# Optimization experiments

Measured on AMD Instinct MI355X. Metric: run time of the kernel, lower is better.

The kernel has to match this reference:

```python
import jax, jax.numpy as jnp
import numpy as np

NUM_NETWORKS = 1024
IN_FEATURES = 32
OUT_FEATURES = 32
POINTS_PER_NET = 128
TOTAL_POINTS = NUM_NETWORKS * POINTS_PER_NET  # 131072


def setup_inputs() -> dict:
    key = jax.random.key(0)
    k1, k2, k3 = jax.random.split(key, 3)
    x = jax.random.normal(k1, (TOTAL_POINTS, IN_FEATURES), dtype=jnp.float32)
    # per-network weight matrices [N, in, out] and biases [N, out]
    weights = jax.random.normal(k2, (NUM_NETWORKS, IN_FEATURES, OUT_FEATURES), dtype=jnp.float32) * 0.1
    biases = jax.random.normal(k3, (NUM_NETWORKS, OUT_FEATURES), dtype=jnp.float32) * 0.1
    # contiguous point counts per network (static/uniform here, matching sum == TOTAL_POINTS)
    batch_size_per_network = jnp.full((NUM_NETWORKS,), POINTS_PER_NET, dtype=jnp.int32)
    return {"x": x, "weights": weights, "biases": biases,
            "batch_size_per_network": batch_size_per_network}


def reference(x, weights, biases, batch_size_per_network):
    # Grouped batched matmul: points are laid out contiguously per network.
    # seg[t] = network id owning point t.
    n = weights.shape[0]
    total = x.shape[0]
    seg = jnp.repeat(jnp.arange(n, dtype=jnp.int32), batch_size_per_network,
                     total_repeat_length=total)  # [total]
    # y_t = x_t @ W[seg_t] + b[seg_t]
    w_t = weights[seg]                     # [total, in, out] (gathered per point)
    y = jnp.einsum('ti,tio->to', x, w_t) + biases[seg]
    return y
```

## Files before the change

### kernel.cpp

```cpp
#include <hip/hip_runtime.h>


#define NT 64

__global__ __launch_bounds__(NT) void mnl_kernel(
    const float* __restrict__ x,
    const float* __restrict__ w,
    const float* __restrict__ bias,
    const int* __restrict__ cnt,
    float* __restrict__ y)
{
    __shared__ float xT[32][NT];
    __shared__ float Wl[32][32];

    const int b = blockIdx.x;
    const int n = b >> 1;
    const int h = b & 1;
    const int t = threadIdx.x;

    const float4* __restrict__ wg = reinterpret_cast<const float4*>(w + (size_t)n * 1024);
    const float4 wr0 = wg[t];
    const float4 wr1 = wg[t + 64];
    const float4 wr2 = wg[t + 128];
    const float4 wr3 = wg[t + 192];

    const int o0 = (t & 7) * 4;
    const int p0 = (t >> 3) * 8;

    const float4 b4 = *reinterpret_cast<const float4*>(bias + (size_t)n * 32 + o0);

    int s = 0;
    for (int j = t; j < n; j += NT) s += cnt[j];
    #pragma unroll
    for (int off = 32; off > 0; off >>= 1) s += __shfl_xor(s, off, 64);
    const int base  = s;
    const int count = cnt[n];

    {
        float4* wl4 = reinterpret_cast<float4*>(&Wl[0][0]);
        wl4[t]       = wr0;
        wl4[t + 64]  = wr1;
        wl4[t + 128] = wr2;
        wl4[t + 192] = wr3;
    }

    for (int pc = h * NT; pc < count; pc += 2 * NT) {
        const int p = pc + t;
        float4 rr[8];
        if (p < count) {
            const float4* __restrict__ xg =
                reinterpret_cast<const float4*>(x + (size_t)(base + p) * 32);
            #pragma unroll
            for (int k = 0; k < 8; ++k) rr[k] = xg[k];
        } else {
            #pragma unroll
            for (int k = 0; k < 8; ++k) rr[k] = make_float4(0.f, 0.f, 0.f, 0.f);
        }

        __syncthreads();

        #pragma unroll
        for (int k = 0; k < 8; ++k) {
            xT[4 * k + 0][t] = rr[k].x;
            xT[4 * k + 1][t] = rr[k].y;
            xT[4 * k + 2][t] = rr[k].z;
            xT[4 * k + 3][t] = rr[k].w;
        }

        __syncthreads();

        float acc[8][4] = {};
        #pragma unroll
        for (int i = 0; i < 32; ++i) {
            const float4 xa = *reinterpret_cast<const float4*>(&xT[i][p0]);
            const float4 xb = *reinterpret_cast<const float4*>(&xT[i][p0 + 4]);
            const float4 wv = *reinterpret_cast<const float4*>(&Wl[i][o0]);
            const float xs[8] = {xa.x, xa.y, xa.z, xa.w, xb.x, xb.y, xb.z, xb.w};
            const float ws[4] = {wv.x, wv.y, wv.z, wv.w};
            #pragma unroll
            for (int pp = 0; pp < 8; ++pp)
                #pragma unroll
                for (int oo = 0; oo < 4; ++oo)
                    acc[pp][oo] = fmaf(xs[pp], ws[oo], acc[pp][oo]);
        }

        #pragma unroll
        for (int pp = 0; pp < 8; ++pp) {
            const int prow = pc + p0 + pp;
            if (prow < count) {
                float4 o;
                o.x = acc[pp][0] + b4.x;
                o.y = acc[pp][1] + b4.y;
                o.z = acc[pp][2] + b4.z;
                o.w = acc[pp][3] + b4.w;
                *reinterpret_cast<float4*>(&y[(size_t)(base + prow) * 32 + o0]) = o;
            }
        }
    }
}

extern "C" void kernel_launch(void* const* d_in, const int* in_sizes, int n_in,
                              void* d_out, int out_size, void* d_ws, size_t ws_size,
                              hipStream_t stream) {
    const float* x    = (const float*)d_in[0];
    const float* w    = (const float*)d_in[1];
    const float* bias = (const float*)d_in[2];
    const int*   cnt  = (const int*)d_in[3];
    float*       y    = (float*)d_out;
    const int n_nets  = in_sizes[3];

    mnl_kernel<<<2 * n_nets, NT, 0, stream>>>(x, w, bias, cnt, y);
}
```

Before: 19.05 us.

## Split each network across four blocks with 32-point chunks and vectorized prefix sum

Each network's points are now handled by four 64-thread blocks instead of two, each processing 32-point chunks. Two threads share the load of one x row, and each thread computes a 4x4 output tile instead of 8x4, which cuts register use. The prefix-sum over counts now reads int4 values, and the bias is folded into the accumulator initialisation. This adds grid parallelism and occupancy at the cost of more blocks that each redo the weight load and prefix sum.

```diff
diff --git a/kernel.cpp b/kernel.cpp
--- a/kernel.cpp
+++ b/kernel.cpp
@@ -2,6 +2,8 @@
 
 
 #define NT 64
+#define CHUNK 32
+#define SPLIT 4
 
 __global__ __launch_bounds__(NT) void mnl_kernel(
     const float* __restrict__ x,
@@ -10,12 +12,12 @@
     const int* __restrict__ cnt,
     float* __restrict__ y)
 {
-    __shared__ float xT[32][NT];
+    __shared__ float xT[32][CHUNK];
     __shared__ float Wl[32][32];
 
     const int b = blockIdx.x;
-    const int n = b >> 1;
-    const int h = b & 1;
+    const int n = b >> 2;
+    const int q = b & 3;
     const int t = threadIdx.x;
 
     const float4* __restrict__ wg = reinterpret_cast<const float4*>(w + (size_t)n * 1024);
@@ -25,12 +27,18 @@
     const float4 wr3 = wg[t + 192];
 
     const int o0 = (t & 7) * 4;
-    const int p0 = (t >> 3) * 8;
+    const int p0 = (t >> 3) * 4;
 
     const float4 b4 = *reinterpret_cast<const float4*>(bias + (size_t)n * 32 + o0);
 
     int s = 0;
-    for (int j = t; j < n; j += NT) s += cnt[j];
+    const int nf = n & ~3;
+    const int4* __restrict__ c4 = reinterpret_cast<const int4*>(cnt);
+    for (int j = 4 * t; j < nf; j += 4 * NT) {
+        const int4 v = c4[j >> 2];
+        s += v.x + v.y + v.z + v.w;
+    }
+    for (int j = nf + t; j < n; j += NT) s += cnt[j];
     #pragma unroll
     for (int off = 32; off > 0; off >>= 1) s += __shfl_xor(s, off, 64);
     const int base  = s;
@@ -44,57 +52,58 @@
         wl4[t + 192] = wr3;
     }
 
-    for (int pc = h * NT; pc < count; pc += 2 * NT) {
-        const int p = pc + t;
-        float4 rr[8];
-        if (p < count) {
+    const int pr = t >> 1;
+    const int cg = (t & 1) * 4;
+
+    for (int pc = q * CHUNK; pc < count; pc += SPLIT * CHUNK) {
+        float4 rr[4];
+        const int pg = pc + pr;
+        if (pg < count) {
             const float4* __restrict__ xg =
-                reinterpret_cast<const float4*>(x + (size_t)(base + p) * 32);
+                reinterpret_cast<const float4*>(x + (size_t)(base + pg) * 32);
             #pragma unroll
-            for (int k = 0; k < 8; ++k) rr[k] = xg[k];
+            for (int k = 0; k < 4; ++k) rr[k] = xg[cg + k];
         } else {
             #pragma unroll
-            for (int k = 0; k < 8; ++k) rr[k] = make_float4(0.f, 0.f, 0.f, 0.f);
+            for (int k = 0; k < 4; ++k) rr[k] = make_float4(0.f, 0.f, 0.f, 0.f);
         }
 
         __syncthreads();
 
         #pragma unroll
-        for (int k = 0; k < 8; ++k) {
-            xT[4 * k + 0][t] = rr[k].x;
-            xT[4 * k + 1][t] = rr[k].y;
-            xT[4 * k + 2][t] = rr[k].z;
-            xT[4 * k + 3][t] = rr[k].w;
+        for (int k = 0; k < 4; ++k) {
+            const int c = cg + k;
+            xT[4 * c + 0][pr] = rr[k].x;
+            xT[4 * c + 1][pr] = rr[k].y;
+            xT[4 * c + 2][pr] = rr[k].z;
+            xT[4 * c + 3][pr] = rr[k].w;
         }
 
         __syncthreads();
 
-        float acc[8][4] = {};
+        float4 acc[4];
+        #pragma unroll
+        for (int pp = 0; pp < 4; ++pp) acc[pp] = b4;
+
         #pragma unroll
         for (int i = 0; i < 32; ++i) {
-            const float4 xa = *reinterpret_cast<const float4*>(&xT[i][p0]);
-            const float4 xb = *reinterpret_cast<const float4*>(&xT[i][p0 + 4]);
+            const float4 xv = *reinterpret_cast<const float4*>(&xT[i][p0]);
             const float4 wv = *reinterpret_cast<const float4*>(&Wl[i][o0]);
-            const float xs[8] = {xa.x, xa.y, xa.z, xa.w, xb.x, xb.y, xb.z, xb.w};
-            const float ws[4] = {wv.x, wv.y, wv.z, wv.w};
+            const float xs[4] = {xv.x, xv.y, xv.z, xv.w};
             #pragma unroll
-            for (int pp = 0; pp < 8; ++pp)
-                #pragma unroll
-                for (int oo = 0; oo < 4; ++oo)
-                    acc[pp][oo] = fmaf(xs[pp], ws[oo], acc[pp][oo]);
+            for (int pp = 0; pp < 4; ++pp) {
+                acc[pp].x = fmaf(xs[pp], wv.x, acc[pp].x);
+                acc[pp].y = fmaf(xs[pp], wv.y, acc[pp].y);
+                acc[pp].z = fmaf(xs[pp], wv.z, acc[pp].z);
+                acc[pp].w = fmaf(xs[pp], wv.w, acc[pp].w);
+            }
         }
 
         #pragma unroll
-        for (int pp = 0; pp < 8; ++pp) {
+        for (int pp = 0; pp < 4; ++pp) {
             const int prow = pc + p0 + pp;
-            if (prow < count) {
-                float4 o;
-                o.x = acc[pp][0] + b4.x;
-                o.y = acc[pp][1] + b4.y;
-                o.z = acc[pp][2] + b4.z;
-                o.w = acc[pp][3] + b4.w;
-                *reinterpret_cast<float4*>(&y[(size_t)(base + prow) * 32 + o0]) = o;
-            }
+            if (prow < count)
+                *reinterpret_cast<float4*>(&y[(size_t)(base + prow) * 32 + o0]) = acc[pp];
         }
     }
 }
@@ -109,5 +118,5 @@
     float*       y    = (float*)d_out;
     const int n_nets  = in_sizes[3];
 
-    mnl_kernel<<<2 * n_nets, NT, 0, stream>>>(x, w, bias, cnt, y);
+    mnl_kernel<<<SPLIT * n_nets, NT, 0, stream>>>(x, w, bias, cnt, y);
 }
```

Result: slower. 22.05 us (+15.8%).
